# Optimization experiments

Hardware: AMD Instinct MI355X
Metric: run time of the kernel (lower is better)

Reference implementation:

```python
import jax, jax.numpy as jnp
import numpy as np

B, S, D, E, N = 2, 1024, 1024, 64, 16  # batch, seq, model_dim, embedding_dim, num_splats


def setup_inputs() -> dict:
    key = jax.random.key(0)
    ks = jax.random.split(key, 8)
    inv_sqrt_d = 1.0 / np.sqrt(D)
    return {
        "token_embeddings": jax.random.normal(ks[0], (B, S, D), jnp.float32),
        # position encoder Linear(D, E)
        "pos_W": jax.random.normal(ks[1], (D, E), jnp.float32) * inv_sqrt_d,
        "pos_b": jnp.zeros((E,), jnp.float32),
        "positional_bias": jax.random.normal(ks[2], (1024, E), jnp.float32) * 0.01,
        "splat_positions": jax.random.normal(ks[3], (N, E), jnp.float32) * 0.2,
        "splat_log_scales": jnp.zeros((N,), jnp.float32),
        # q/k/v Linear(D, D, bias=False)
        "q_W": jax.random.normal(ks[4], (D, D), jnp.float32) * inv_sqrt_d,
        "k_W": jax.random.normal(ks[5], (D, D), jnp.float32) * inv_sqrt_d,
        "v_W": jax.random.normal(ks[6], (D, D), jnp.float32) * inv_sqrt_d,
        "splat_gates": jnp.full((N,), 0.5, jnp.float32),
        "residual_weight": jnp.asarray(0.8, jnp.float32),
        "ln_w": jnp.ones((D,), jnp.float32),
        "ln_b": jnp.zeros((D,), jnp.float32),
    }


def reference(token_embeddings, pos_W, pos_b, positional_bias, splat_positions,
              splat_log_scales, q_W, k_W, v_W, splat_gates, residual_weight,
              ln_w, ln_b):
    b, s, d = token_embeddings.shape
    # token positions in splat embedding space: tanh(Linear(x)) + pos_bias[:S]
    positions = jnp.tanh(token_embeddings @ pos_W + pos_b) + positional_bias[:s][None]  # [B,S,E]
    # spatial influence per splat: Gaussian of distance, clamped scales, floor 0.01
    diff = positions[:, :, None, :] - splat_positions[None, None]  # [B,S,N,E]
    dist_sq = jnp.sum(diff * diff, axis=-1)                         # [B,S,N]
    scales = jnp.clip(jnp.exp(splat_log_scales), 0.3, 2.0)
    influence = jnp.maximum(jnp.exp(-0.5 * dist_sq / (scales * scales)), 0.01)  # [B,S,N]

    q = token_embeddings @ q_W
    k = token_embeddings @ k_W
    v = token_embeddings @ v_W

    w = jnp.transpose(influence, (2, 0, 1))      # [N,B,S]
    qw = q[None] * w[..., None]                  # [N,B,S,D]
    kw = k[None] * w[..., None]
    scores = jnp.einsum('nbid,nbjd->nbij', qw, kw) / jnp.sqrt(jnp.asarray(d, jnp.float32))
    causal = jnp.tril(jnp.ones((s, s), bool))
    scores = jnp.where(causal[None, None], scores, -1e9)
    attn = jax.nn.softmax(scores, axis=-1)       # [N,B,S,S]
    out = jnp.einsum('nbij,bjd->nbid', attn, v)  # [N,B,S,D]

    gates = jax.nn.sigmoid(splat_gates)[:, None, None, None]
    combined = jnp.mean(out * gates, axis=0)     # [B,S,D]

    rw = jax.nn.sigmoid(residual_weight)
    o = rw * token_embeddings + (1.0 - rw) * combined
    # LayerNorm (eps=1e-5)
    mu = jnp.mean(o, axis=-1, keepdims=True)
    var = jnp.mean((o - mu) ** 2, axis=-1, keepdims=True)
    return (o - mu) / jnp.sqrt(var + 1e-5) * ln_w + ln_b
```

## Files before the change

### kernel.cpp

```cpp
#include <hip/hip_runtime.h>
#include <hip/hip_bf16.h>
#include <hip/hip_fp16.h>

using bf16 = __hip_bfloat16;
typedef __attribute__((ext_vector_type(8))) short short8;
typedef __attribute__((ext_vector_type(4))) float f32x4;

static constexpr int Bb = 2, Ss = 1024, Dd = 1024, Ee = 64, Nn = 16;

struct Params {
    const float *X, *posW, *posB, *pbias, *spos, *lsc, *qW, *kW, *vW, *gates, *rwp, *lnw, *lnb;
    bf16 *Xb, *Wt, *WpT, *QKV, *Vt, *Aav;
    __half *wh;
    float *qk0, *qk1, *cb0, *cb1, *out;
};

__device__ __forceinline__ unsigned short f2bfr(float f) {
    __hip_bfloat16 h = __float2bfloat16(f);
    return *reinterpret_cast<unsigned short*>(&h);
}

#define GL_LDS(gp, lp) __builtin_amdgcn_global_load_lds( \
    (const __attribute__((address_space(1))) void*)(gp), \
    (__attribute__((address_space(3))) void*)(lp), 16, 0, 0)

__device__ __forceinline__ void do_transpose_f2b(
    const float* __restrict__ in, bf16* __restrict__ out,
    int R, int C, int bx, int by, char* sm)
{
    float (*tile)[65] = (float(*)[65])sm;
    int tx = threadIdx.x & 63, ty = threadIdx.x >> 6;
    int r0 = by * 64, c0 = bx * 64;
    #pragma unroll
    for (int i = 0; i < 16; ++i)
        tile[ty + i*4][tx] = in[(long)(r0 + ty + i*4)*C + c0 + tx];
    __syncthreads();
    #pragma unroll
    for (int i = 0; i < 16; ++i)
        out[(long)(c0 + ty + i*4)*R + r0 + tx] = __float2bfloat16(tile[tx][ty + i*4]);
    __syncthreads();
}

__device__ __forceinline__ void do_gemm64(
    const bf16* __restrict__ Ab, const bf16* __restrict__ Bw, float* __restrict__ C,
    int Nc, int m0, int n0, int kBeg, int kEnd, float scale, char* sm)
{
    short* lA = (short*)sm;
    short* lB = (short*)(sm + 8192);
    int tid = threadIdx.x, wid = tid >> 6, lane = tid & 63;
    int wn = wid * 32, r16 = lane & 15, quad = lane >> 4;

    f32x4 acc[4][2];
    #pragma unroll
    for (int i = 0; i < 4; ++i)
        #pragma unroll
        for (int j = 0; j < 2; ++j)
            #pragma unroll
            for (int c = 0; c < 4; ++c) acc[i][j][c] = 0.f;

    const short* Ag = (const short*)Ab;
    const short* Bg = (const short*)Bw;

    int arow[2], akg[2], brow[4], bkg[4];
    #pragma unroll
    for (int j = 0; j < 2; ++j) {
        int c = tid + j*256; arow[j] = c >> 3; akg[j] = (c & 7) ^ (arow[j] & 7);
    }
    #pragma unroll
    for (int j = 0; j < 4; ++j) {
        int c = tid + j*256; brow[j] = c >> 3; bkg[j] = (c & 7) ^ (brow[j] & 7);
    }

    for (int k0 = kBeg; k0 < kEnd; k0 += 64) {
        __syncthreads();
        #pragma unroll
        for (int j = 0; j < 2; ++j)
            GL_LDS(Ag + (long)(m0 + arow[j])*1024 + k0 + akg[j]*8, lA + (tid + j*256)*8);
        #pragma unroll
        for (int j = 0; j < 4; ++j)
            GL_LDS(Bg + (long)(n0 + brow[j])*1024 + k0 + bkg[j]*8, lB + (tid + j*256)*8);
        __syncthreads();

        #pragma unroll
        for (int kk = 0; kk < 2; ++kk) {
            int kc = kk*4 + quad;
            short8 af[4], bfv[2];
            #pragma unroll
            for (int i = 0; i < 4; ++i) {
                int r = i*16 + r16;
                af[i] = *(const short8*)(lA + r*64 + (kc ^ (r & 7))*8);
            }
            #pragma unroll
            for (int j = 0; j < 2; ++j) {
                int r = wn + j*16 + r16;
                bfv[j] = *(const short8*)(lB + r*64 + (kc ^ (r & 7))*8);
            }
            #pragma unroll
            for (int i = 0; i < 4; ++i)
                #pragma unroll
                for (int j = 0; j < 2; ++j)
                    acc[i][j] = __builtin_amdgcn_mfma_f32_16x16x32_bf16(af[i], bfv[j], acc[i][j], 0, 0, 0);
        }
    }

    #pragma unroll
    for (int i = 0; i < 4; ++i)
        #pragma unroll
        for (int j = 0; j < 2; ++j)
            #pragma unroll
            for (int rr = 0; rr < 4; ++rr)
                C[(long)(m0 + i*16 + quad*4 + rr)*Nc + n0 + wn + j*16 + r16] =
                    acc[i][j][rr] * scale;
}

template<int OUT_MODE>
__device__ __forceinline__ void do_gemm128(
    const bf16* __restrict__ Ab, const bf16* __restrict__ Bw, void* __restrict__ Cv,
    int Nc, int m0, int n0, char* sm)
{
    short* lA = (short*)sm;
    short* lB = (short*)(sm + 16384);
    int tid = threadIdx.x, wid = tid >> 6, lane = tid & 63;
    int wm = (wid >> 1) * 64, wnn = (wid & 1) * 64;
    int r16 = lane & 15, quad = lane >> 4;

    f32x4 acc[4][4];
    #pragma unroll
    for (int i = 0; i < 4; ++i)
        #pragma unroll
        for (int j = 0; j < 4; ++j)
            #pragma unroll
            for (int c = 0; c < 4; ++c) acc[i][j][c] = 0.f;

    const short* Ag = (const short*)Ab;
    const short* Bg = (const short*)Bw;

    int rowc[4], kgc[4];
    #pragma unroll
    for (int j = 0; j < 4; ++j) {
        int c = tid + j*256; rowc[j] = c >> 3; kgc[j] = (c & 7) ^ (rowc[j] & 7);
    }

    for (int k0 = 0; k0 < 1024; k0 += 64) {
        __syncthreads();
        #pragma unroll
        for (int j = 0; j < 4; ++j)
            GL_LDS(Ag + (long)(m0 + rowc[j])*1024 + k0 + kgc[j]*8, lA + (tid + j*256)*8);
        #pragma unroll
        for (int j = 0; j < 4; ++j)
            GL_LDS(Bg + (long)(n0 + rowc[j])*1024 + k0 + kgc[j]*8, lB + (tid + j*256)*8);
        __syncthreads();

        #pragma unroll
        for (int kk = 0; kk < 2; ++kk) {
            int kc = kk*4 + quad;
            short8 af[4], bfv[4];
            #pragma unroll
            for (int i = 0; i < 4; ++i) {
                int r = wm + i*16 + r16;
                af[i] = *(const short8*)(lA + r*64 + (kc ^ (r & 7))*8);
            }
            #pragma unroll
            for (int j = 0; j < 4; ++j) {
                int r = wnn + j*16 + r16;
                bfv[j] = *(const short8*)(lB + r*64 + (kc ^ (r & 7))*8);
            }
            #pragma unroll
            for (int i = 0; i < 4; ++i)
                #pragma unroll
                for (int j = 0; j < 4; ++j)
                    acc[i][j] = __builtin_amdgcn_mfma_f32_16x16x32_bf16(af[i], bfv[j], acc[i][j], 0, 0, 0);
        }
    }

    if (OUT_MODE == 1) {
        bf16* C = (bf16*)Cv;
        #pragma unroll
        for (int i = 0; i < 4; ++i)
            #pragma unroll
            for (int j = 0; j < 4; ++j)
                #pragma unroll
                for (int rr = 0; rr < 4; ++rr)
                    C[(long)(m0 + wm + i*16 + quad*4 + rr)*Nc + n0 + wnn + j*16 + r16] =
                        __float2bfloat16(acc[i][j][rr]);
    } else {
        __syncthreads();
        bf16 (*lt)[132] = (bf16(*)[132])sm;
        #pragma unroll
        for (int i = 0; i < 4; ++i)
            #pragma unroll
            for (int j = 0; j < 4; ++j)
                #pragma unroll
                for (int rr = 0; rr < 4; ++rr)
                    lt[wnn + j*16 + r16][wm + i*16 + quad*4 + rr] =
                        __float2bfloat16(acc[i][j][rr]);
        __syncthreads();
        bf16* Vb = (bf16*)Cv + (long)(m0 >> 10) * Dd * Ss;
        int s0 = m0 & (Ss - 1);
        int colBase = wid * 32 + (lane >> 4);
        int idx = (lane & 15) * 8;
        #pragma unroll
        for (int it = 0; it < 8; ++it) {
            int col = colBase + it * 4;
            ushort4 v0 = *(const ushort4*)&lt[col][idx];
            ushort4 v1 = *(const ushort4*)&lt[col][idx + 4];
            *(ushort4*)(Vb + (long)(n0 + col)*Ss + s0 + idx)     = v0;
            *(ushort4*)(Vb + (long)(n0 + col)*Ss + s0 + idx + 4) = v1;
        }
    }
}

__device__ __forceinline__ void do_pos(const Params& p, int m0, char* sm)
{
    short* lA = (short*)sm;
    short* lB = (short*)(sm + 4096);
    float (*P)[65]  = (float(*)[65])(sm + 8192);
    float (*sp)[65] = (float(*)[65])(sm + 8192 + 64*65*4);

    int tid = threadIdx.x, wid = tid >> 6, lane = tid & 63;
    int r16 = lane & 15, quad = lane >> 4;

    for (int idx = tid; idx < 16*64; idx += 256)
        sp[idx >> 6][idx & 63] = p.spos[idx];

    f32x4 acc[4];
    #pragma unroll
    for (int j = 0; j < 4; ++j)
        #pragma unroll
        for (int c = 0; c < 4; ++c) acc[j][c] = 0.f;

    int ra = tid >> 2, ka = (tid & 3) * 8;
    const short* Ag = (const short*)p.Xb;
    const short* Bg = (const short*)p.WpT;

    for (int k0 = 0; k0 < Dd; k0 += 32) {
        __syncthreads();
        GL_LDS(Ag + (long)(m0+ra)*1024 + k0 + ka, lA + tid*8);
        GL_LDS(Bg + (long)ra*1024 + k0 + ka,      lB + tid*8);
        __syncthreads();

        short8 af = *(const short8*)(lA + (wid*16 + r16)*32 + quad*8);
        #pragma unroll
        for (int j = 0; j < 4; ++j) {
            short8 bfv = *(const short8*)(lB + (j*16 + r16)*32 + quad*8);
            acc[j] = __builtin_amdgcn_mfma_f32_16x16x32_bf16(af, bfv, acc[j], 0, 0, 0);
        }
    }

    #pragma unroll
    for (int j = 0; j < 4; ++j)
        #pragma unroll
        for (int rr = 0; rr < 4; ++rr) {
            int rl  = wid*16 + quad*4 + rr;
            int col = j*16 + r16;
            int srow = (m0 + rl) & (Ss - 1);
            P[rl][col] = tanhf(acc[j][rr] + p.posB[col]) + p.pbias[srow*Ee + col];
        }
    __syncthreads();

    int n  = tid & 15;
    int rb = (tid >> 4) * 4;
    float sc = __expf(p.lsc[n]);
    sc = fminf(fmaxf(sc, 0.3f), 2.0f);
    float inv2 = -0.5f / (sc * sc);
    #pragma unroll
    for (int rr = 0; rr < 4; ++rr) {
        int row = rb + rr;
        float d2 = 0.f;
        #pragma unroll 16
        for (int e = 0; e < 64; ++e) {
            float df = P[row][e] - sp[n][e];
            d2 += df * df;
        }
        float infl = fmaxf(__expf(d2 * inv2), 0.01f);
        p.wh[(long)(m0 + row)*Nn + n] = __float2half(infl);
    }
}

__global__ __launch_bounds__(256) void k_prep(Params p)
{
    __shared__ __align__(16) char sm[64*65*4];
    int z = blockIdx.z;
    if (z < 3) {
        const float* w = (z == 0) ? p.qW : (z == 1) ? p.kW : p.vW;
        do_transpose_f2b(w, p.Wt + (long)z*Dd*Dd, Dd, Dd, blockIdx.x, blockIdx.y, sm);
    } else if (blockIdx.x == 0) {
        do_transpose_f2b(p.posW, p.WpT, Dd, Ee, 0, blockIdx.y, sm);
    } else {
        int job = blockIdx.y * 15 + (blockIdx.x - 1);
        const float4* src = (const float4*)p.X;
        ushort4* dst = (ushort4*)p.Xb;
        for (int idx = job*256 + (int)threadIdx.x; idx < Bb*Ss*Dd/4; idx += 240*256) {
            float4 v = src[idx];
            ushort4 y;
            y.x = f2bfr(v.x); y.y = f2bfr(v.y); y.z = f2bfr(v.z); y.w = f2bfr(v.w);
            dst[idx] = y;
        }
    }
}

__global__ __launch_bounds__(256) void k_qkv_pos(Params p)
{
    __shared__ __align__(16) char sm[33792];
    int job = blockIdx.x;
    if (job < 384) {
        int z = job >> 7, t = job & 127;
        int bm = t >> 3, bn = t & 7;
        if (z < 2)
            do_gemm128<1>(p.Xb, p.Wt + (long)z*Dd*Dd, p.QKV + (long)z*2048*1024,
                          Dd, bm*128, bn*128, sm);
        else
            do_gemm128<2>(p.Xb, p.Wt + (long)2*Dd*Dd, p.Vt,
                          Dd, bm*128, bn*128, sm);
    } else {
        do_pos(p, (job - 384)*64, sm);
    }
}

__global__ __launch_bounds__(256) void k_qkt(Params p)
{
    __shared__ __align__(16) char sm[24576];
    int job = blockIdx.x;
    int pairIdx = job >> 1, h = job & 1;
    int b = pairIdx / 72, t = pairIdx % 72;
    int acc = 0, bm = 0, bn = 0;
    #pragma unroll
    for (int u = 0; u < 16; ++u) {
        int c = (u >> 1) + 1;
        if (t < acc + c) { bm = u; bn = t - acc; break; }
        acc += c;
    }
    const bf16* Qb = p.QKV + (long)b*Ss*Dd;
    const bf16* Kb = p.QKV + (long)2048*1024 + (long)b*Ss*Dd;
    float* dst = (h ? p.qk1 : p.qk0) + (long)b*Ss*Ss;
    do_gemm64(Qb, Kb, dst, Ss, bm*64, bn*128, h*512, h*512 + 512, 0.03125f, sm);
}

__global__ __launch_bounds__(256) void k_softmax(Params p)
{
    __shared__ __align__(16) char sm[36864 + 256];
    __half2 (*wt)[9] = (__half2(*)[9])sm;
    float (*wi4)[16] = (float(*)[16])(sm + 36864);

    int base = blockIdx.x * 4, b = blockIdx.y;
    int tid = threadIdx.x, wid = tid >> 6, lane = tid & 63;
    int imax = base + 3;

    const __half*  whb  = p.wh + (long)b*Ss*Nn;
    const __half2* whb2 = (const __half2*)whb;

    for (int j = tid; j <= imax; j += 256) {
        #pragma unroll
        for (int h = 0; h < 8; ++h)
            wt[j][h] = whb2[j*8 + h];
    }
    if (tid < 64) wi4[tid >> 4][tid & 15] =
        __half2float(whb[(long)(base + (tid >> 4))*16 + (tid & 15)]);
    __syncthreads();

    int i = base + wid;
    const float* q0 = p.qk0 + ((long)b*Ss + i)*Ss;
    const float* q1 = p.qk1 + ((long)b*Ss + i)*Ss;
    bf16* arow      = p.Aav + ((long)b*Ss + i)*Ss;

    float wiR[16], l[16], qv[16];
    #pragma unroll
    for (int n = 0; n < 16; ++n) { wiR[n] = wi4[wid][n]; l[n] = 0.f; }

    #pragma unroll
    for (int t = 0; t < 16; ++t) {
        int j = lane + 64*t;
        if (j <= i) {
            float q = q0[j] + q1[j];
            qv[t] = q;
            #pragma unroll
            for (int h = 0; h < 8; ++h) {
                float2 f = __half22float2(wt[j][h]);
                l[2*h]     += __expf(wiR[2*h]     * f.x * q);
                l[2*h + 1] += __expf(wiR[2*h + 1] * f.y * q);
            }
        }
    }
    #pragma unroll
    for (int n = 0; n < 16; ++n)
        #pragma unroll
        for (int off = 32; off > 0; off >>= 1)
            l[n] += __shfl_xor(l[n], off);

    float coef[16];
    #pragma unroll
    for (int n = 0; n < 16; ++n) {
        float g  = p.gates[n];
        float sg = 1.f / (1.f + __expf(-g));
        coef[n]  = sg / (16.f * l[n]);
    }

    #pragma unroll
    for (int t = 0; t < 16; ++t) {
        int j = lane + 64*t;
        float a = 0.f;
        if (j <= i) {
            float q = qv[t];
            #pragma unroll
            for (int h = 0; h < 8; ++h) {
                float2 f = __half22float2(wt[j][h]);
                a += coef[2*h]     * __expf(wiR[2*h]     * f.x * q);
                a += coef[2*h + 1] * __expf(wiR[2*h + 1] * f.y * q);
            }
        }
        arow[j] = __float2bfloat16(a);
    }
}

__global__ __launch_bounds__(256) void k_av(Params p)
{
    __shared__ __align__(16) char sm[24576];
    int job = blockIdx.x;
    int b, bm, bn, kBeg, kEnd;
    if (job < 256) {
        b = job >> 7; int t = job & 127; bm = t >> 3; bn = t & 7;
        kBeg = 0; kEnd = bm*64 + 64; if (kEnd > 512) kEnd = 512;
    } else {
        int j = job - 256;
        b = j >> 6; int t = j & 63; bm = 8 + (t >> 3); bn = t & 7;
        kBeg = 512; kEnd = bm*64 + 64;
    }
    const bf16* Ab = p.Aav + (long)b*Ss*Ss;
    const bf16* Bw = p.Vt + (long)b*Dd*Ss;
    float* dst = (job < 256 ? p.cb0 : p.cb1) + (long)b*Ss*Dd;
    do_gemm64(Ab, Bw, dst, Dd, bm*64, bn*128, kBeg, kEnd, 1.f, sm);
}

__global__ __launch_bounds__(256) void k_epilogue(Params p)
{
    __shared__ float rs[4], rq[4];
    long row = blockIdx.x;
    int tid = threadIdx.x, wid = tid >> 6, lane = tid & 63;
    float rw = 1.f / (1.f + __expf(-p.rwp[0]));

    float4 c0 = ((const float4*)(p.cb0 + row*Dd))[tid];
    int s = (int)(row & (Ss - 1));
    float4 c1 = make_float4(0.f, 0.f, 0.f, 0.f);
    if (s >= 512) c1 = ((const float4*)(p.cb1 + row*Dd))[tid];
    float4 xv = ((const float4*)(p.X + row*Dd))[tid];

    float o[4];
    o[0] = rw * xv.x + (1.f - rw) * (c0.x + c1.x);
    o[1] = rw * xv.y + (1.f - rw) * (c0.y + c1.y);
    o[2] = rw * xv.z + (1.f - rw) * (c0.z + c1.z);
    o[3] = rw * xv.w + (1.f - rw) * (c0.w + c1.w);

    float sm1 = o[0] + o[1] + o[2] + o[3];
    float sq  = o[0]*o[0] + o[1]*o[1] + o[2]*o[2] + o[3]*o[3];
    #pragma unroll
    for (int off = 32; off > 0; off >>= 1) { sm1 += __shfl_xor(sm1, off); sq += __shfl_xor(sq, off); }
    if (lane == 0) { rs[wid] = sm1; rq[wid] = sq; }
    __syncthreads();
    sm1 = rs[0] + rs[1] + rs[2] + rs[3];
    sq  = rq[0] + rq[1] + rq[2] + rq[3];
    float mu  = sm1 * (1.f/1024.f);
    float var = sq * (1.f/1024.f) - mu*mu;
    float inv = rsqrtf(var + 1e-5f);

    float4 lw = ((const float4*)p.lnw)[tid];
    float4 lb = ((const float4*)p.lnb)[tid];
    float4 y;
    y.x = (o[0] - mu)*inv*lw.x + lb.x;
    y.y = (o[1] - mu)*inv*lw.y + lb.y;
    y.z = (o[2] - mu)*inv*lw.z + lb.z;
    y.w = (o[3] - mu)*inv*lw.w + lb.w;
    ((float4*)(p.out + row*Dd))[tid] = y;
}

extern "C" void kernel_launch(void* const* d_in, const int* in_sizes, int n_in,
                              void* d_out, int out_size, void* d_ws, size_t ws_size,
                              hipStream_t stream)
{
    Params prm;
    prm.X     = (const float*)d_in[0];
    prm.posW  = (const float*)d_in[1];
    prm.posB  = (const float*)d_in[2];
    prm.pbias = (const float*)d_in[3];
    prm.spos  = (const float*)d_in[4];
    prm.lsc   = (const float*)d_in[5];
    prm.qW    = (const float*)d_in[6];
    prm.kW    = (const float*)d_in[7];
    prm.vW    = (const float*)d_in[8];
    prm.gates = (const float*)d_in[9];
    prm.rwp   = (const float*)d_in[10];
    prm.lnw   = (const float*)d_in[11];
    prm.lnb   = (const float*)d_in[12];

    char* ws = (char*)d_ws;
    size_t off = 0;
    prm.Xb  = (bf16*)(ws + off);   off += (size_t)Bb*Ss*Dd*2;
    prm.Wt  = (bf16*)(ws + off);   off += (size_t)3*Dd*Dd*2;
    prm.WpT = (bf16*)(ws + off);   off += (size_t)Ee*Dd*2;
    prm.QKV = (bf16*)(ws + off);   off += (size_t)2*2048*1024*2;
    prm.Vt  = (bf16*)(ws + off);   off += (size_t)Bb*Dd*Ss*2;
    prm.Aav = (bf16*)(ws + off);   off += (size_t)Bb*Ss*Ss*2;
    prm.wh  = (__half*)(ws + off); off += (size_t)Bb*Ss*Nn*2;
    prm.qk0 = (float*)(ws + off);  off += (size_t)Bb*Ss*Ss*4;
    prm.qk1 = (float*)(ws + off);  off += (size_t)Bb*Ss*Ss*4;
    prm.cb0 = (float*)(ws + off);  off += (size_t)Bb*Ss*Dd*4;
    prm.cb1 = (float*)(ws + off);  off += (size_t)Bb*Ss*Dd*4;
    prm.out = (float*)d_out;
    (void)ws_size;

    k_prep    <<<dim3(16,16,4), 256, 0, stream>>>(prm);
    k_qkv_pos <<<416,            256, 0, stream>>>(prm);
    k_qkt     <<<288,            256, 0, stream>>>(prm);
    k_softmax <<<dim3(256, 2),   256, 0, stream>>>(prm);
    k_av      <<<384,            256, 0, stream>>>(prm);
    k_epilogue<<<2048,           256, 0, stream>>>(prm);
}
```

Measured before the change: 166.3 us.

## Fuse fp32-to-bf16 conversion and weight transpose into QKV and position GEMM loads

Removes the separate prep kernel that converted X to bf16 and transposed the q/k/v/pos weights into bf16 workspace buffers. The GEMMs now read fp32 X and untransposed fp32 weights directly, convert them to bf16 in registers and write them into swizzled LDS (weights transposed on the fly as packed k-pairs), with a new swizzle function. This saves a kernel launch and a round trip of the converted data through global memory. In exchange, each GEMM tile reads twice as many bytes as fp32, repeats the conversion for every tile that uses the same data, and gives up the async global_load_lds path for register-staged loads.

```diff
diff --git a/kernel.cpp b/kernel.cpp
--- a/kernel.cpp
+++ b/kernel.cpp
@@ -10,7 +10,7 @@
 
 struct Params {
     const float *X, *posW, *posB, *pbias, *spos, *lsc, *qW, *kW, *vW, *gates, *rwp, *lnw, *lnb;
-    bf16 *Xb, *Wt, *WpT, *QKV, *Vt, *Aav;
+    bf16 *QKV, *Vt, *Aav;
     __half *wh;
     float *qk0, *qk1, *cb0, *cb1, *out;
 };
@@ -19,27 +19,14 @@
     __hip_bfloat16 h = __float2bfloat16(f);
     return *reinterpret_cast<unsigned short*>(&h);
 }
+__device__ __forceinline__ unsigned pk2(float a, float b) {
+    return ((unsigned)f2bfr(b) << 16) | (unsigned)f2bfr(a);
+}
+__device__ __forceinline__ int swz(int r) { return (r ^ (r >> 3)) & 7; }
 
 #define GL_LDS(gp, lp) __builtin_amdgcn_global_load_lds( \
     (const __attribute__((address_space(1))) void*)(gp), \
     (__attribute__((address_space(3))) void*)(lp), 16, 0, 0)
-
-__device__ __forceinline__ void do_transpose_f2b(
-    const float* __restrict__ in, bf16* __restrict__ out,
-    int R, int C, int bx, int by, char* sm)
-{
-    float (*tile)[65] = (float(*)[65])sm;
-    int tx = threadIdx.x & 63, ty = threadIdx.x >> 6;
-    int r0 = by * 64, c0 = bx * 64;
-    #pragma unroll
-    for (int i = 0; i < 16; ++i)
-        tile[ty + i*4][tx] = in[(long)(r0 + ty + i*4)*C + c0 + tx];
-    __syncthreads();
-    #pragma unroll
-    for (int i = 0; i < 16; ++i)
-        out[(long)(c0 + ty + i*4)*R + r0 + tx] = __float2bfloat16(tile[tx][ty + i*4]);
-    __syncthreads();
-}
 
 __device__ __forceinline__ void do_gemm64(
     const bf16* __restrict__ Ab, const bf16* __restrict__ Bw, float* __restrict__ C,
@@ -114,8 +101,8 @@
 }
 
 template<int OUT_MODE>
-__device__ __forceinline__ void do_gemm128(
-    const bf16* __restrict__ Ab, const bf16* __restrict__ Bw, void* __restrict__ Cv,
+__device__ __forceinline__ void do_gemm128f(
+    const float* __restrict__ Af, const float* __restrict__ Wf, void* __restrict__ Cv,
     int Nc, int m0, int n0, char* sm)
 {
     short* lA = (short*)sm;
@@ -132,23 +119,35 @@
             #pragma unroll
             for (int c = 0; c < 4; ++c) acc[i][j][c] = 0.f;
 
-    const short* Ag = (const short*)Ab;
-    const short* Bg = (const short*)Bw;
-
-    int rowc[4], kgc[4];
-    #pragma unroll
-    for (int j = 0; j < 4; ++j) {
-        int c = tid + j*256; rowc[j] = c >> 3; kgc[j] = (c & 7) ^ (rowc[j] & 7);
-    }
+    int am = tid >> 1, ak = (tid & 1) * 32;
+    int brp = tid >> 3, bc = (tid & 7) * 16;
+    int bkch = brp >> 2, bkoff = (2*brp) & 7;
 
     for (int k0 = 0; k0 < 1024; k0 += 64) {
         __syncthreads();
         #pragma unroll
-        for (int j = 0; j < 4; ++j)
-            GL_LDS(Ag + (long)(m0 + rowc[j])*1024 + k0 + kgc[j]*8, lA + (tid + j*256)*8);
-        #pragma unroll
-        for (int j = 0; j < 4; ++j)
-            GL_LDS(Bg + (long)(n0 + rowc[j])*1024 + k0 + kgc[j]*8, lB + (tid + j*256)*8);
+        for (int it = 0; it < 8; ++it) {
+            int k = ak + it*4;
+            float4 v = *(const float4*)(Af + (long)(m0 + am)*1024 + k0 + k);
+            int addr = am*64 + (((k >> 3) ^ swz(am)) * 8) + (k & 7);
+            *(unsigned*)(lA + addr)     = pk2(v.x, v.y);
+            *(unsigned*)(lA + addr + 2) = pk2(v.z, v.w);
+        }
+        #pragma unroll
+        for (int it = 0; it < 4; ++it) {
+            int c = bc + it*4;
+            const float* w0 = Wf + (long)(k0 + 2*brp)*1024 + n0 + c;
+            float4 r0 = *(const float4*)w0;
+            float4 r1 = *(const float4*)(w0 + 1024);
+            float a0[4] = {r0.x, r0.y, r0.z, r0.w};
+            float a1[4] = {r1.x, r1.y, r1.z, r1.w};
+            #pragma unroll
+            for (int i = 0; i < 4; ++i) {
+                int n = c + i;
+                int addr = n*64 + ((bkch ^ swz(n)) * 8) + bkoff;
+                *(unsigned*)(lB + addr) = pk2(a0[i], a1[i]);
+            }
+        }
         __syncthreads();
 
         #pragma unroll
@@ -158,12 +157,12 @@
             #pragma unroll
             for (int i = 0; i < 4; ++i) {
                 int r = wm + i*16 + r16;
-                af[i] = *(const short8*)(lA + r*64 + (kc ^ (r & 7))*8);
+                af[i] = *(const short8*)(lA + r*64 + (kc ^ swz(r))*8);
             }
             #pragma unroll
             for (int j = 0; j < 4; ++j) {
                 int r = wnn + j*16 + r16;
-                bfv[j] = *(const short8*)(lB + r*64 + (kc ^ (r & 7))*8);
+                bfv[j] = *(const short8*)(lB + r*64 + (kc ^ swz(r))*8);
             }
             #pragma unroll
             for (int i = 0; i < 4; ++i)
@@ -210,12 +209,12 @@
     }
 }
 
-__device__ __forceinline__ void do_pos(const Params& p, int m0, char* sm)
+__device__ __forceinline__ void do_pos32(const Params& p, int m0, char* sm)
 {
     short* lA = (short*)sm;
-    short* lB = (short*)(sm + 4096);
-    float (*P)[65]  = (float(*)[65])(sm + 8192);
-    float (*sp)[65] = (float(*)[65])(sm + 8192 + 64*65*4);
+    short* lB = (short*)(sm + 8192);
+    float (*P)[65]  = (float(*)[65])(sm + 16384);
+    float (*sp)[65] = (float(*)[65])(sm + 16384 + 16640);
 
     int tid = threadIdx.x, wid = tid >> 6, lane = tid & 63;
     int r16 = lane & 15, quad = lane >> 4;
@@ -229,21 +228,48 @@
         #pragma unroll
         for (int c = 0; c < 4; ++c) acc[j][c] = 0.f;
 
-    int ra = tid >> 2, ka = (tid & 3) * 8;
-    const short* Ag = (const short*)p.Xb;
-    const short* Bg = (const short*)p.WpT;
-
-    for (int k0 = 0; k0 < Dd; k0 += 32) {
-        __syncthreads();
-        GL_LDS(Ag + (long)(m0+ra)*1024 + k0 + ka, lA + tid*8);
-        GL_LDS(Bg + (long)ra*1024 + k0 + ka,      lB + tid*8);
-        __syncthreads();
-
-        short8 af = *(const short8*)(lA + (wid*16 + r16)*32 + quad*8);
-        #pragma unroll
-        for (int j = 0; j < 4; ++j) {
-            short8 bfv = *(const short8*)(lB + (j*16 + r16)*32 + quad*8);
-            acc[j] = __builtin_amdgcn_mfma_f32_16x16x32_bf16(af, bfv, acc[j], 0, 0, 0);
+    int am = tid >> 2, ak = (tid & 3) * 16;
+    int brp = tid >> 3, bc = (tid & 7) * 8;
+    int bkch = brp >> 2, bkoff = (2*brp) & 7;
+
+    for (int k0 = 0; k0 < 1024; k0 += 64) {
+        __syncthreads();
+        #pragma unroll
+        for (int it = 0; it < 4; ++it) {
+            int k = ak + it*4;
+            float4 v = *(const float4*)(p.X + (long)(m0 + am)*1024 + k0 + k);
+            int addr = am*64 + (((k >> 3) ^ swz(am)) * 8) + (k & 7);
+            *(unsigned*)(lA + addr)     = pk2(v.x, v.y);
+            *(unsigned*)(lA + addr + 2) = pk2(v.z, v.w);
+        }
+        #pragma unroll
+        for (int it = 0; it < 2; ++it) {
+            int c = bc + it*4;
+            const float* w0 = p.posW + (long)(k0 + 2*brp)*Ee + c;
+            float4 r0 = *(const float4*)w0;
+            float4 r1 = *(const float4*)(w0 + Ee);
+            float a0[4] = {r0.x, r0.y, r0.z, r0.w};
+            float a1[4] = {r1.x, r1.y, r1.z, r1.w};
+            #pragma unroll
+            for (int i = 0; i < 4; ++i) {
+                int n = c + i;
+                int addr = n*64 + ((bkch ^ swz(n)) * 8) + bkoff;
+                *(unsigned*)(lB + addr) = pk2(a0[i], a1[i]);
+            }
+        }
+        __syncthreads();
+
+        #pragma unroll
+        for (int kk = 0; kk < 2; ++kk) {
+            int kc = kk*4 + quad;
+            int ra = wid*16 + r16;
+            short8 af = *(const short8*)(lA + ra*64 + (kc ^ swz(ra))*8);
+            #pragma unroll
+            for (int j = 0; j < 4; ++j) {
+                int r = j*16 + r16;
+                short8 bfv = *(const short8*)(lB + r*64 + (kc ^ swz(r))*8);
+                acc[j] = __builtin_amdgcn_mfma_f32_16x16x32_bf16(af, bfv, acc[j], 0, 0, 0);
+            }
         }
     }
 
@@ -277,43 +303,20 @@
     }
 }
 
-__global__ __launch_bounds__(256) void k_prep(Params p)
-{
-    __shared__ __align__(16) char sm[64*65*4];
-    int z = blockIdx.z;
-    if (z < 3) {
-        const float* w = (z == 0) ? p.qW : (z == 1) ? p.kW : p.vW;
-        do_transpose_f2b(w, p.Wt + (long)z*Dd*Dd, Dd, Dd, blockIdx.x, blockIdx.y, sm);
-    } else if (blockIdx.x == 0) {
-        do_transpose_f2b(p.posW, p.WpT, Dd, Ee, 0, blockIdx.y, sm);
-    } else {
-        int job = blockIdx.y * 15 + (blockIdx.x - 1);
-        const float4* src = (const float4*)p.X;
-        ushort4* dst = (ushort4*)p.Xb;
-        for (int idx = job*256 + (int)threadIdx.x; idx < Bb*Ss*Dd/4; idx += 240*256) {
-            float4 v = src[idx];
-            ushort4 y;
-            y.x = f2bfr(v.x); y.y = f2bfr(v.y); y.z = f2bfr(v.z); y.w = f2bfr(v.w);
-            dst[idx] = y;
-        }
-    }
-}
-
 __global__ __launch_bounds__(256) void k_qkv_pos(Params p)
 {
-    __shared__ __align__(16) char sm[33792];
+    __shared__ __align__(16) char sm[37184];
     int job = blockIdx.x;
     if (job < 384) {
         int z = job >> 7, t = job & 127;
         int bm = t >> 3, bn = t & 7;
+        const float* Wf = (z == 0) ? p.qW : (z == 1) ? p.kW : p.vW;
         if (z < 2)
-            do_gemm128<1>(p.Xb, p.Wt + (long)z*Dd*Dd, p.QKV + (long)z*2048*1024,
-                          Dd, bm*128, bn*128, sm);
+            do_gemm128f<1>(p.X, Wf, p.QKV + (long)z*2048*1024, Dd, bm*128, bn*128, sm);
         else
-            do_gemm128<2>(p.Xb, p.Wt + (long)2*Dd*Dd, p.Vt,
-                          Dd, bm*128, bn*128, sm);
+            do_gemm128f<2>(p.X, Wf, p.Vt, Dd, bm*128, bn*128, sm);
     } else {
-        do_pos(p, (job - 384)*64, sm);
+        do_pos32(p, (job - 384)*64, sm);
     }
 }
 
@@ -493,9 +496,6 @@
 
     char* ws = (char*)d_ws;
     size_t off = 0;
-    prm.Xb  = (bf16*)(ws + off);   off += (size_t)Bb*Ss*Dd*2;
-    prm.Wt  = (bf16*)(ws + off);   off += (size_t)3*Dd*Dd*2;
-    prm.WpT = (bf16*)(ws + off);   off += (size_t)Ee*Dd*2;
     prm.QKV = (bf16*)(ws + off);   off += (size_t)2*2048*1024*2;
     prm.Vt  = (bf16*)(ws + off);   off += (size_t)Bb*Dd*Ss*2;
     prm.Aav = (bf16*)(ws + off);   off += (size_t)Bb*Ss*Ss*2;
@@ -507,10 +507,9 @@
     prm.out = (float*)d_out;
     (void)ws_size;
 
-    k_prep    <<<dim3(16,16,4), 256, 0, stream>>>(prm);
-    k_qkv_pos <<<416,            256, 0, stream>>>(prm);
-    k_qkt     <<<288,            256, 0, stream>>>(prm);
-    k_softmax <<<dim3(256, 2),   256, 0, stream>>>(prm);
-    k_av      <<<384,            256, 0, stream>>>(prm);
-    k_epilogue<<<2048,           256, 0, stream>>>(prm);
-}
+    k_qkv_pos <<<416,          256, 0, stream>>>(prm);
+    k_qkt     <<<288,          256, 0, stream>>>(prm);
+    k_softmax <<<dim3(256, 2), 256, 0, stream>>>(prm);
+    k_av      <<<384,          256, 0, stream>>>(prm);
+    k_epilogue<<<2048,         256, 0, stream>>>(prm);
+}
```

Result: slower. 182.6 us (+9.8%).
